# Kernel tuning notes

Measured on AMD Instinct MI355X. Metric: run time of the kernel, lower is better.

Reference implementation:

```python
import jax, jax.numpy as jnp
import numpy as np


def setup_inputs() -> dict:
    key = jax.random.key(0)
    N, E, H, V, C, D, L = 10000, 50000, 128, 8, 5, 59, 2
    keys = iter(jax.random.split(key, 64))

    def p(*shape):
        return jax.random.normal(next(keys), shape, jnp.float32) * 0.05

    inp = dict(
        edge_index=jax.random.randint(next(keys), (2, E), 0, N),
        edge_attr=jax.random.normal(next(keys), (E, D), jnp.float32),
        delta_t=jnp.array([60.0], jnp.float32),
        memory=jnp.ones((N, H), jnp.float32),
        # edge_embed
        W_ee=p(H, D), b_ee=p(H),
        # edge_weight_gen
        W_ewg=p(V, 2 * H), b_ewg=p(V),
        # multi-view GIN convs (L layers, shared MLP across views)
        gin_W1=p(L, H, H), gin_b1=p(L, H), gin_W2=p(L, H, H), gin_b2=p(L, H),
        # Bochner time encoder
        W_t=p(H, 1), b_t=p(H),
        # GRUCell (torch gate order r,z,n)
        W_ih=p(3 * H, H), b_ih=p(3 * H), W_hh=p(3 * H, H), b_hh=p(3 * H),
        # update_nn (feeds detached memory only; not in returned outputs)
        W_up=p(H, V * H), b_up=p(H),
        # local attention (kdim=vdim=2H, 1 head)
        Wq_l=p(H, H), bq_l=p(H), Wk_l=p(H, 2 * H), bk_l=p(H),
        Wv_l=p(H, 2 * H), bv_l=p(H), Wo_l=p(H, H), bo_l=p(H),
        # global attention (1 head)
        Wq_g=p(H, H), bq_g=p(H), Wk_g=p(H, H), bk_g=p(H),
        Wv_g=p(H, H), bv_g=p(H), Wo_g=p(H, H), bo_g=p(H),
        # classifier MLP
        Wc1=p(H, 3 * H), bc1=p(H), Wc2=p(C, H), bc2=p(C),
    )
    return inp


def reference(edge_index, edge_attr, delta_t, memory,
              W_ee, b_ee, W_ewg, b_ewg,
              gin_W1, gin_b1, gin_W2, gin_b2,
              W_t, b_t, W_ih, b_ih, W_hh, b_hh, W_up, b_up,
              Wq_l, bq_l, Wk_l, bk_l, Wv_l, bv_l, Wo_l, bo_l,
              Wq_g, bq_g, Wk_g, bk_g, Wv_g, bv_g, Wo_g, bo_g,
              Wc1, bc1, Wc2, bc2):
    relu = jax.nn.relu
    N, H = memory.shape
    V = W_ewg.shape[0]
    L = gin_W1.shape[0]

    # ---- snapshot encoder (MultiGraphLayer) ----
    ea = relu(edge_attr @ W_ee.T + b_ee)                               # [E,H]
    src0, dst0 = edge_index[0], edge_index[1]
    ew = jax.nn.sigmoid(
        jnp.concatenate([ea, memory[src0]], -1) @ W_ewg.T + b_ewg)     # [E,V]
    h = jnp.broadcast_to(memory[:, None, :], (N, V, H))                # [N,V,H]
    cs, cd = dst0, src0  # edge_index flipped before convs (edge_index[[1,0]])
    for l in range(L):
        # multi-view GIN: view-weighted message + residual MLP update
        msg = relu(h[cs] + ea[:, None, :]) * ew[:, :, None]            # [E,V,H]
        agg = jax.ops.segment_sum(msg, cd, num_segments=N)             # [N,V,H]
        upd = relu((h + agg) @ gin_W1[l].T + gin_b1[l]) @ gin_W2[l].T + gin_b2[l]
        h = h + upd
    h_before = h

    # ---- GRU memory update (vectorized over the V 'class' slots) ----
    te = jnp.sin(delta_t[:, None] * W_t[:, 0] + b_t)                   # [1,H]
    x_in = h + te                                                      # [N,V,H]
    gi = x_in @ W_ih.T + b_ih                                          # [N,V,3H]
    gh = (memory @ W_hh.T + b_hh)[:, None, :]                          # [N,1,3H]
    r = jax.nn.sigmoid(gi[..., :H] + gh[..., :H])
    z = jax.nn.sigmoid(gi[..., H:2 * H] + gh[..., H:2 * H])
    n = jnp.tanh(gi[..., 2 * H:] + r * gh[..., 2 * H:])
    h_new = (1.0 - z) * n + z * memory[:, None, :]                     # [N,V,H]

    # ---- global/local attention fusion ----
    scale = 1.0 / jnp.sqrt(jnp.asarray(H, jnp.float32))
    sf, df = h_new[src0], h_new[dst0]                                  # [E,V,H]
    Wk1, Wk2 = Wk_l[:, :H], Wk_l[:, H:]  # split cat([src,dst]) projection
    Wv1, Wv2 = Wv_l[:, :H], Wv_l[:, H:]
    q_l = ea @ Wq_l.T + bq_l                                           # [E,H]
    K_l = sf @ Wk1.T + df @ Wk2.T + bk_l                               # [E,V,H]
    V_l = sf @ Wv1.T + df @ Wv2.T + bv_l
    a_l = jax.nn.softmax(jnp.einsum('eh,evh->ev', q_l, K_l) * scale, -1)
    local_out = jnp.einsum('ev,evh->eh', a_l, V_l) @ Wo_l.T + bo_l     # [E,H]

    pooled = h_new.mean(axis=0)                                        # [V,H]
    q_g = ea @ Wq_g.T + bq_g
    K_g = pooled @ Wk_g.T + bk_g
    V_g = pooled @ Wv_g.T + bv_g
    a_g = jax.nn.softmax((q_g @ K_g.T) * scale, axis=-1)               # [E,V]
    global_out = (a_g @ V_g) @ Wo_g.T + bo_g                           # [E,H]

    combined = jnp.concatenate([ea, local_out, global_out], axis=-1)   # [E,3H]
    logits = relu(combined @ Wc1.T + bc1) @ Wc2.T + bc2                # [E,C]
    return (logits, ew, h_before, a_g[:, None, :])
```

## Files before the change

kernel.cpp:

```cpp
#include <hip/hip_runtime.h>
#include <cstddef>


#define HSZ 128
typedef unsigned short ushortT;
typedef unsigned int uintT;
typedef short short8 __attribute__((ext_vector_type(8)));
typedef float f32x4 __attribute__((ext_vector_type(4)));

__device__ __forceinline__ float sigm(float x) { return 1.f / (1.f + __expf(-x)); }

__device__ __forceinline__ ushortT f2bf(float f) {
  unsigned int u = __float_as_uint(f);
  u += 0x7fffu + ((u >> 16) & 1u);
  return (ushortT)(u >> 16);
}
__device__ __forceinline__ float bf2f(ushortT u) {
  return __uint_as_float(((unsigned int)u) << 16);
}
__device__ __forceinline__ float bflo(uintT u) { return __uint_as_float(u << 16); }
__device__ __forceinline__ float bfhi(uintT u) { return __uint_as_float(u & 0xffff0000u); }
__device__ __forceinline__ uintT pk2bf(float a, float b) {
  return ((uintT)f2bf(b) << 16) | (uintT)f2bf(a);
}

__device__ __forceinline__ int swzA(int row, int chunk) {
  return row * 64 + (((chunk ^ row) & 7) << 3);
}
__device__ __forceinline__ int swzT(int row, int chunk) {
  return row * 128 + (((chunk & 8) | ((chunk ^ row) & 7)) << 3);
}

template<int ASRC, int ACT, bool OUTBF, bool ABF, bool WBF>
__global__ __launch_bounds__(256) void gemm_bf(
    const void* __restrict__ A1, const void* __restrict__ A2, const void* __restrict__ A3,
    const void* __restrict__ W, const float* __restrict__ bias,
    void* __restrict__ out_, int M, int K, int Nout)
{
  __shared__ short Ash[128 * 64];
  __shared__ short Bsh[128 * 64];
  float* out = (float*)out_;
  ushortT* outh = (ushortT*)out_;
  const int tid = threadIdx.x;
  const int m0 = blockIdx.x * 128;
  const int n0 = blockIdx.y * 128;
  const int l = tid & 63, w = tid >> 6;
  const int wr = w >> 1, wc = w & 1;
  const int lr = l & 15, lq = l >> 4;
  f32x4 acc[4][4] = {};

  for (int k0 = 0; k0 < K; k0 += 64) {
    __syncthreads();
    const bool fast = (k0 + 64 <= K);
    #pragma unroll
    for (int i = 0; i < 4; ++i) {
      int c = i * 256 + tid;
      int row = c >> 3, seg = c & 7;
      int kb = k0 + seg * 8;
      {
        int m = m0 + row;
        short8 pk;
        if (ABF) {
          if (m < M) {
            if (ASRC == 4) {
              if (kb < 128)
                pk = *reinterpret_cast<const short8*>((const ushortT*)A1 + (size_t)m * 128 + kb);
              else if (kb < 384)
                pk = *reinterpret_cast<const short8*>((const ushortT*)A2 + (size_t)m * 256 + (kb - 128));
              else
                pk = *reinterpret_cast<const short8*>((const ushortT*)A3 + (size_t)m * 128 + (kb - 384));
            } else {
              pk = *reinterpret_cast<const short8*>((const ushortT*)A1 + (size_t)m * K + kb);
            }
          } else {
            #pragma unroll
            for (int j = 0; j < 8; ++j) pk[j] = 0;
          }
        } else {
          const float* A1f = (const float*)A1;
          float v[8];
          if (fast && m < M) {
            const float4* p = reinterpret_cast<const float4*>(A1f + (size_t)m * K + kb);
            float4 x0 = p[0], x1 = p[1];
            v[0]=x0.x; v[1]=x0.y; v[2]=x0.z; v[3]=x0.w;
            v[4]=x1.x; v[5]=x1.y; v[6]=x1.z; v[7]=x1.w;
          } else {
            #pragma unroll
            for (int j = 0; j < 8; ++j) {
              int k = kb + j;
              v[j] = (m < M && k < K) ? A1f[(size_t)m * K + k] : 0.f;
            }
          }
          #pragma unroll
          for (int j = 0; j < 8; ++j) pk[j] = (short)f2bf(v[j]);
        }
        *reinterpret_cast<short8*>(&Ash[swzA(row, seg)]) = pk;
      }
      {
        int nn = n0 + row;
        short8 pk;
        if (WBF) {
          if (nn < Nout)
            pk = *reinterpret_cast<const short8*>((const ushortT*)W + (size_t)nn * K + kb);
          else {
            #pragma unroll
            for (int j = 0; j < 8; ++j) pk[j] = 0;
          }
        } else {
          const float* Wf = (const float*)W;
          float v[8];
          if (fast && nn < Nout) {
            const float4* p = reinterpret_cast<const float4*>(Wf + (size_t)nn * K + kb);
            float4 x0 = p[0], x1 = p[1];
            v[0]=x0.x; v[1]=x0.y; v[2]=x0.z; v[3]=x0.w;
            v[4]=x1.x; v[5]=x1.y; v[6]=x1.z; v[7]=x1.w;
          } else {
            #pragma unroll
            for (int j = 0; j < 8; ++j) {
              int k = kb + j;
              v[j] = (nn < Nout && k < K) ? Wf[(size_t)nn * K + k] : 0.f;
            }
          }
          #pragma unroll
          for (int j = 0; j < 8; ++j) pk[j] = (short)f2bf(v[j]);
        }
        *reinterpret_cast<short8*>(&Bsh[swzA(row, seg)]) = pk;
      }
    }
    __syncthreads();
    #pragma unroll
    for (int ks = 0; ks < 2; ++ks) {
      short8 a[4], b[4];
      #pragma unroll
      for (int mi = 0; mi < 4; ++mi)
        a[mi] = *reinterpret_cast<const short8*>(&Ash[swzA(wr*64 + mi*16 + lr, ks*4 + lq)]);
      #pragma unroll
      for (int ni = 0; ni < 4; ++ni)
        b[ni] = *reinterpret_cast<const short8*>(&Bsh[swzA(wc*64 + ni*16 + lr, ks*4 + lq)]);
      #pragma unroll
      for (int mi = 0; mi < 4; ++mi)
        #pragma unroll
        for (int ni = 0; ni < 4; ++ni)
          acc[mi][ni] = __builtin_amdgcn_mfma_f32_16x16x32_bf16(a[mi], b[ni], acc[mi][ni], 0, 0, 0);
    }
  }
  #pragma unroll
  for (int ni = 0; ni < 4; ++ni) {
    int col = n0 + wc*64 + ni*16 + lr;
    if (col >= Nout) continue;
    float bz = bias ? bias[col] : 0.f;
    #pragma unroll
    for (int mi = 0; mi < 4; ++mi) {
      int mb = m0 + wr*64 + mi*16 + lq*4;
      #pragma unroll
      for (int r = 0; r < 4; ++r) {
        int m = mb + r;
        if (m >= M) continue;
        float vv = acc[mi][ni][r] + bz;
        if (ACT == 1) vv = fmaxf(vv, 0.f);
        size_t o = (size_t)m * Nout + col;
        if (OUTBF) outh[o] = f2bf(vv); else out[o] = vv;
      }
    }
  }
}

template<int LMODE>
__global__ __launch_bounds__(256) void k_gin(
    const ushortT* __restrict__ hb, const ushortT* __restrict__ aggb,
    float* __restrict__ houtf, ushortT* __restrict__ houtb,
    const ushortT* __restrict__ W1b, const float* __restrict__ b1,
    const ushortT* __restrict__ W2b, const float* __restrict__ b2, int M)
{
  __shared__ short smem[24576];
  short* Ash  = smem;
  short* Bsh  = smem + 8192;
  short* Tsh  = smem;
  short* B2sh = smem + 16384;
  const int tid = threadIdx.x;
  const int m0 = blockIdx.x * 128;
  const int l = tid & 63, w = tid >> 6;
  const int wr = w >> 1, wc = w & 1;
  const int lr = l & 15, lq = l >> 4;
  f32x4 acc[4][4] = {};

  for (int ks2 = 0; ks2 < 2; ++ks2) {
    if (ks2) __syncthreads();
    #pragma unroll
    for (int i = 0; i < 4; ++i) {
      int c = i * 256 + tid;
      int row = c >> 3, seg = c & 7;
      int kb = ks2 * 64 + seg * 8;
      {
        int m = m0 + row;
        short8 pk;
        if (m < M) {
          short8 hv;
          if (LMODE == 1) hv = *reinterpret_cast<const short8*>(hb + ((size_t)(m >> 3)) * 128 + kb);
          else            hv = *reinterpret_cast<const short8*>(hb + (size_t)m * 128 + kb);
          short8 av = *reinterpret_cast<const short8*>(aggb + (size_t)m * 128 + kb);
          #pragma unroll
          for (int j = 0; j < 8; ++j)
            pk[j] = (short)f2bf(bf2f((ushortT)hv[j]) + bf2f((ushortT)av[j]));
        } else {
          #pragma unroll
          for (int j = 0; j < 8; ++j) pk[j] = 0;
        }
        *reinterpret_cast<short8*>(&Ash[swzA(row, seg)]) = pk;
      }
      *reinterpret_cast<short8*>(&Bsh[swzA(row, seg)]) =
          *reinterpret_cast<const short8*>(W1b + (size_t)row * 128 + kb);
      if (ks2 == 0)
        *reinterpret_cast<short8*>(&B2sh[swzA(row, seg)]) =
            *reinterpret_cast<const short8*>(W2b + (size_t)row * 128 + seg * 8);
    }
    __syncthreads();
    #pragma unroll
    for (int ks = 0; ks < 2; ++ks) {
      short8 a[4], b[4];
      #pragma unroll
      for (int mi = 0; mi < 4; ++mi)
        a[mi] = *reinterpret_cast<const short8*>(&Ash[swzA(wr*64 + mi*16 + lr, ks*4 + lq)]);
      #pragma unroll
      for (int ni = 0; ni < 4; ++ni)
        b[ni] = *reinterpret_cast<const short8*>(&Bsh[swzA(wc*64 + ni*16 + lr, ks*4 + lq)]);
      #pragma unroll
      for (int mi = 0; mi < 4; ++mi)
        #pragma unroll
        for (int ni = 0; ni < 4; ++ni)
          acc[mi][ni] = __builtin_amdgcn_mfma_f32_16x16x32_bf16(a[mi], b[ni], acc[mi][ni], 0, 0, 0);
    }
  }
  __syncthreads();
  {
    float b1v[4];
    #pragma unroll
    for (int ni = 0; ni < 4; ++ni) b1v[ni] = b1[wc*64 + ni*16 + lr];
    #pragma unroll
    for (int mi = 0; mi < 4; ++mi)
      #pragma unroll
      for (int ni = 0; ni < 4; ++ni) {
        int col = wc*64 + ni*16 + lr;
        #pragma unroll
        for (int r = 0; r < 4; ++r) {
          int row = wr*64 + mi*16 + lq*4 + r;
          float v = fmaxf(acc[mi][ni][r] + b1v[ni], 0.f);
          Tsh[swzT(row, col >> 3) + (col & 7)] = (short)f2bf(v);
        }
      }
  }
  __syncthreads();
  f32x4 acc2[4][4] = {};
  for (int ks2 = 0; ks2 < 2; ++ks2) {
    if (ks2) {
      __syncthreads();
      #pragma unroll
      for (int i = 0; i < 4; ++i) {
        int c = i * 256 + tid;
        int row = c >> 3, seg = c & 7;
        *reinterpret_cast<short8*>(&B2sh[swzA(row, seg)]) =
            *reinterpret_cast<const short8*>(W2b + (size_t)row * 128 + 64 + seg * 8);
      }
      __syncthreads();
    }
    #pragma unroll
    for (int ks = 0; ks < 2; ++ks) {
      short8 a[4], b[4];
      #pragma unroll
      for (int mi = 0; mi < 4; ++mi)
        a[mi] = *reinterpret_cast<const short8*>(&Tsh[swzT(wr*64 + mi*16 + lr, ks2*8 + ks*4 + lq)]);
      #pragma unroll
      for (int ni = 0; ni < 4; ++ni)
        b[ni] = *reinterpret_cast<const short8*>(&B2sh[swzA(wc*64 + ni*16 + lr, ks*4 + lq)]);
      #pragma unroll
      for (int mi = 0; mi < 4; ++mi)
        #pragma unroll
        for (int ni = 0; ni < 4; ++ni)
          acc2[mi][ni] = __builtin_amdgcn_mfma_f32_16x16x32_bf16(a[mi], b[ni], acc2[mi][ni], 0, 0, 0);
    }
  }
  {
    float b2v[4];
    #pragma unroll
    for (int ni = 0; ni < 4; ++ni) b2v[ni] = b2[wc*64 + ni*16 + lr];
    #pragma unroll
    for (int ni = 0; ni < 4; ++ni) {
      int col = wc*64 + ni*16 + lr;
      #pragma unroll
      for (int mi = 0; mi < 4; ++mi) {
        int mb = m0 + wr*64 + mi*16 + lq*4;
        #pragma unroll
        for (int r = 0; r < 4; ++r) {
          int m = mb + r;
          if (m >= M) continue;
          float base = (LMODE == 1) ? bf2f(hb[((size_t)(m >> 3)) * 128 + col])
                                    : bf2f(hb[(size_t)m * 128 + col]);
          float ho = base + acc2[mi][ni][r] + b2v[ni];
          if (LMODE == 1) houtb[(size_t)m * 128 + col] = f2bf(ho);
          else            houtf[(size_t)m * 128 + col] = ho;
        }
      }
    }
  }
}

__global__ __launch_bounds__(512) void k_giru(
    const float* __restrict__ hf, const float* __restrict__ te,
    const ushortT* __restrict__ Wihb, const float* __restrict__ b_ih,
    const ushortT* __restrict__ ghb, const ushortT* __restrict__ memb,
    ushortT* __restrict__ hnb, float* __restrict__ prw, int M)
{
  __shared__ short Ash[8192];
  __shared__ short Bsh[24576];
  float* poolsh = reinterpret_cast<float*>(Ash);
  const int tid = threadIdx.x;
  const int m0 = blockIdx.x * 64;
  const int l = tid & 63, w = tid >> 6;
  const int lr = l & 15, lq = l >> 4;
  const int r0 = (w >> 1) * 16, c0 = (w & 1) * 64;
  f32x4 acc[3][4] = {};

  #pragma unroll
  for (int i = 0; i < 2; ++i) {
    int c = i * 512 + tid;
    int row = c >> 4, seg = c & 15;
    int m = m0 + row;
    short8 pk;
    if (m < M) {
      const float4* p = reinterpret_cast<const float4*>(hf + (size_t)m * 128 + seg * 8);
      const float4* t = reinterpret_cast<const float4*>(te + seg * 8);
      float4 x0 = p[0], x1 = p[1], t0 = t[0], t1 = t[1];
      pk[0]=(short)f2bf(x0.x+t0.x); pk[1]=(short)f2bf(x0.y+t0.y);
      pk[2]=(short)f2bf(x0.z+t0.z); pk[3]=(short)f2bf(x0.w+t0.w);
      pk[4]=(short)f2bf(x1.x+t1.x); pk[5]=(short)f2bf(x1.y+t1.y);
      pk[6]=(short)f2bf(x1.z+t1.z); pk[7]=(short)f2bf(x1.w+t1.w);
    } else {
      #pragma unroll
      for (int j = 0; j < 8; ++j) pk[j] = 0;
    }
    *reinterpret_cast<short8*>(&Ash[swzT(row, seg)]) = pk;
  }
  for (int ks2 = 0; ks2 < 2; ++ks2) {
    if (ks2) __syncthreads();
    #pragma unroll
    for (int i = 0; i < 6; ++i) {
      int c = i * 512 + tid;
      int row = c >> 3, seg = c & 7;
      *reinterpret_cast<short8*>(&Bsh[swzA(row, seg)]) =
          *reinterpret_cast<const short8*>(Wihb + (size_t)row * 128 + ks2 * 64 + seg * 8);
    }
    __syncthreads();
    #pragma unroll
    for (int ks = 0; ks < 2; ++ks) {
      short8 a = *reinterpret_cast<const short8*>(&Ash[swzT(r0 + lr, ks2*8 + ks*4 + lq)]);
      #pragma unroll
      for (int s = 0; s < 3; ++s)
        #pragma unroll
        for (int xi = 0; xi < 4; ++xi) {
          short8 b = *reinterpret_cast<const short8*>(
              &Bsh[swzA(s*128 + c0 + xi*16 + lr, ks*4 + lq)]);
          acc[s][xi] = __builtin_amdgcn_mfma_f32_16x16x32_bf16(a, b, acc[s][xi], 0, 0, 0);
        }
    }
  }
  __syncthreads();
  for (int i = tid; i < 1024; i += 512) poolsh[i] = 0.f;
  __syncthreads();
  #pragma unroll
  for (int xi = 0; xi < 4; ++xi) {
    int x = c0 + xi * 16 + lr;
    float br = b_ih[x], bz = b_ih[128 + x], bn = b_ih[256 + x];
    #pragma unroll
    for (int rr = 0; rr < 4; ++rr) {
      int m = m0 + r0 + lq * 4 + rr;
      if (m >= M) continue;
      int node = m >> 3;
      float ghr = bf2f(ghb[(size_t)node * 384 + x]);
      float ghz = bf2f(ghb[(size_t)node * 384 + 128 + x]);
      float ghn = bf2f(ghb[(size_t)node * 384 + 256 + x]);
      float mem = bf2f(memb[(size_t)node * 128 + x]);
      float rv = sigm(acc[0][xi][rr] + br + ghr);
      float zv = sigm(acc[1][xi][rr] + bz + ghz);
      float nv = tanhf(acc[2][xi][rr] + bn + rv * ghn);
      float hn = (1.f - zv) * nv + zv * mem;
      hnb[(size_t)m * 128 + x] = f2bf(hn);
      atomicAdd(&poolsh[(m & 7) * 128 + x], hn);
    }
  }
  __syncthreads();
  for (int i = tid; i < 1024; i += 512) atomicAdd(&prw[i], poolsh[i]);
}

__global__ void k_hist(const int* __restrict__ srcI, int* __restrict__ cnt, int E)
{
  int e = blockIdx.x * 256 + threadIdx.x;
  if (e < E) atomicAdd(&cnt[srcI[e]], 1);
}

__global__ __launch_bounds__(1024) void k_scan(const int* __restrict__ cnt,
    int* __restrict__ ofs, int* __restrict__ cur, int N)
{
  __shared__ int buf[1024];
  __shared__ int carry;
  int tid = threadIdx.x;
  if (tid == 0) carry = 0;
  __syncthreads();
  for (int base = 0; base < N; base += 1024) {
    int i = base + tid;
    int v = (i < N) ? cnt[i] : 0;
    buf[tid] = v;
    __syncthreads();
    for (int off = 1; off < 1024; off <<= 1) {
      int t = (tid >= off) ? buf[tid - off] : 0;
      __syncthreads();
      buf[tid] += t;
      __syncthreads();
    }
    int excl = carry + buf[tid] - v;
    if (i < N) { ofs[i] = excl; cur[i] = excl; }
    __syncthreads();
    if (tid == 0) carry += buf[1023];
    __syncthreads();
  }
  if (tid == 0) ofs[N] = carry;
}

__global__ void k_fill(const int* __restrict__ srcI, int* __restrict__ cur,
                       int* __restrict__ eid, int E)
{
  int e = blockIdx.x * 256 + threadIdx.x;
  if (e >= E) return;
  int p = atomicAdd(&cur[srcI[e]], 1);
  eid[p] = e;
}

template<int LMODE>
__global__ __launch_bounds__(256) void k_agg(const ushortT* __restrict__ hb,
    const ushortT* __restrict__ eab, const float* __restrict__ ew,
    const int* __restrict__ dstI, const int* __restrict__ ofs,
    const int* __restrict__ eid, ushortT* __restrict__ aggb, int N)
{
  int half = threadIdx.x >> 7;
  int x = threadIdx.x & 127;
  int n = blockIdx.x * 2 + half;
  if (n >= N) return;
  float acc[8] = {};
  int beg = ofs[n], end = ofs[n + 1];
  for (int i = beg; i < end; ++i) {
    int e = eid[i];
    int d = dstI[e];
    float eav = bf2f(eab[(size_t)e * 128 + x]);
    const float* ewp = ew + (size_t)e * 8;
    if (LMODE == 1) {
      float m = fmaxf(bf2f(hb[(size_t)d * 128 + x]) + eav, 0.f);
      #pragma unroll
      for (int v = 0; v < 8; ++v) acc[v] += m * ewp[v];
    } else {
      const ushortT* hd = hb + (size_t)d * 1024;
      #pragma unroll
      for (int v = 0; v < 8; ++v)
        acc[v] += fmaxf(bf2f(hd[v * 128 + x]) + eav, 0.f) * ewp[v];
    }
  }
  ushortT* ag = aggb + (size_t)n * 1024;
  #pragma unroll
  for (int v = 0; v < 8; ++v) ag[v * 128 + x] = f2bf(acc[v]);
}

__global__ __launch_bounds__(256) void k_ew(const ushortT* __restrict__ eab,
    const ushortT* __restrict__ memb, const int* __restrict__ srcI,
    const float* __restrict__ W_ewg, const float* __restrict__ b_ewg,
    float* __restrict__ ew, int E)
{
  __shared__ float Wsh[2048];
  __shared__ float bsh[8];
  int tid = threadIdx.x;
  for (int i = tid; i < 2048; i += 256) Wsh[i] = W_ewg[i];
  if (tid < 8) bsh[tid] = b_ewg[tid];
  __syncthreads();
  int wv = tid >> 6, lane = tid & 63;
  int e = blockIdx.x * 4 + wv;
  if (e >= E) return;
  int s = srcI[e];
  float c0 = bf2f(eab[(size_t)e * 128 + lane]);
  float c1 = bf2f(eab[(size_t)e * 128 + 64 + lane]);
  float c2 = bf2f(memb[(size_t)s * 128 + lane]);
  float c3 = bf2f(memb[(size_t)s * 128 + 64 + lane]);
  #pragma unroll
  for (int v = 0; v < 8; ++v) {
    float p = c0 * Wsh[v * 256 + lane] + c1 * Wsh[v * 256 + 64 + lane]
            + c2 * Wsh[v * 256 + 128 + lane] + c3 * Wsh[v * 256 + 192 + lane];
    #pragma unroll
    for (int o = 32; o; o >>= 1) p += __shfl_down(p, o);
    if (lane == 0) ew[(size_t)e * 8 + v] = sigm(p + bsh[v]);
  }
}

__global__ void k_cvtall(const float* __restrict__ s0, ushortT* __restrict__ d0, int n0,
                         const float* __restrict__ s1, ushortT* __restrict__ d1, int n1,
                         const float* __restrict__ s2, ushortT* __restrict__ d2, int n2,
                         const float* __restrict__ s3, ushortT* __restrict__ d3, int n3)
{
  int i = blockIdx.x * 256 + threadIdx.x;
  if (i < n0) { d0[i] = f2bf(s0[i]); return; }
  i -= n0;
  if (i < n1) { d1[i] = f2bf(s1[i]); return; }
  i -= n1;
  if (i < n2) { d2[i] = f2bf(s2[i]); return; }
  i -= n2;
  if (i < n3) d3[i] = f2bf(s3[i]);
}

__global__ __launch_bounds__(256) void k_prep(
    const float* __restrict__ Wo_l, const float* __restrict__ Wv_l,
    const float* __restrict__ bv_l, const float* __restrict__ bo_l,
    const float* __restrict__ Wq_l, const float* __restrict__ bq_l,
    const float* __restrict__ Wk_l,
    const float* __restrict__ delta_t, const float* __restrict__ W_t,
    const float* __restrict__ b_t,
    float* __restrict__ Wl2f, float* __restrict__ blv,
    ushortT* __restrict__ Wqkgb, float* __restrict__ bqkg, float* __restrict__ te)
{
  int idx = blockIdx.x * 256 + threadIdx.x;
  if (idx < 32768) {
    int n = idx >> 8, k = idx & 255;
    float a = 0.f;
    for (int j = 0; j < 128; ++j) a += Wo_l[n * 128 + j] * Wv_l[j * 256 + k];
    Wl2f[idx] = a;
  } else {
    int rem = idx - 32768;
    int n = rem >> 7, j = rem & 127;
    float a = 0.f;
    for (int k = 0; k < 128; ++k) a += Wq_l[k * 128 + j] * Wk_l[k * 256 + n];
    Wqkgb[rem] = f2bf(a);
  }
  if (blockIdx.x == 0 && threadIdx.x < 128) {
    int n = threadIdx.x;
    float a = bo_l[n];
    for (int j = 0; j < 128; ++j) a += Wo_l[n * 128 + j] * bv_l[j];
    blv[n] = a;
  }
  if (blockIdx.x == 1) {
    int n = threadIdx.x;
    float a = 0.f;
    for (int k = 0; k < 128; ++k) a += bq_l[k] * Wk_l[k * 256 + n];
    bqkg[n] = a;
  }
  if (blockIdx.x == 2 && threadIdx.x < 128) {
    int t = threadIdx.x;
    te[t] = sinf(delta_t[0] * W_t[t] + b_t[t]);
  }
}

__global__ __launch_bounds__(256) void k_prep2(
    const float* __restrict__ Wc1, const float* __restrict__ bc1,
    const float* __restrict__ Wl2f, const float* __restrict__ blv,
    ushortT* __restrict__ Wc1p, float* __restrict__ bc1p)
{
  int idx = blockIdx.x * 256 + threadIdx.x;
  int n = idx >> 9, k = idx & 511;
  float a;
  if (k < 128) a = Wc1[(size_t)n * 384 + k];
  else if (k < 384) {
    int kk = k - 128;
    a = 0.f;
    for (int j = 0; j < 128; ++j) a += Wc1[(size_t)n * 384 + 128 + j] * Wl2f[j * 256 + kk];
  } else a = Wc1[(size_t)n * 384 + 256 + (k - 384)];
  Wc1p[idx] = f2bf(a);
  if (blockIdx.x == 0 && threadIdx.x < 128) {
    int nn = threadIdx.x;
    float b = bc1[nn];
    for (int j = 0; j < 128; ++j) b += Wc1[(size_t)nn * 384 + 128 + j] * blv[j];
    bc1p[nn] = b;
  }
}

__global__ __launch_bounds__(256) void k_kgg(const float* __restrict__ prw,
    const float* __restrict__ Wk_g, const float* __restrict__ Wv_g, const float* __restrict__ bv_g,
    const float* __restrict__ Wo_g, float* __restrict__ Kg, float* __restrict__ G, int N)
{
  __shared__ float pl[1024];
  __shared__ float vg[1024];
  int tid = threadIdx.x;
  float invN = 1.f / (float)N;
  for (int i = tid; i < 1024; i += 256) pl[i] = prw[i] * invN;
  __syncthreads();
  for (int o = tid; o < 1024; o += 256) {
    int v = o >> 7, x = o & 127;
    float a = 0.f, b = 0.f;
    for (int k = 0; k < 128; ++k) {
      float p = pl[v * 128 + k];
      a += p * Wk_g[(size_t)x * 128 + k];
      b += p * Wv_g[(size_t)x * 128 + k];
    }
    Kg[o] = a;
    vg[o] = b + bv_g[x];
  }
  __syncthreads();
  for (int o = tid; o < 1024; o += 256) {
    int v = o >> 7, x = o & 127;
    float a = 0.f;
    for (int k = 0; k < 128; ++k) a += vg[v * 128 + k] * Wo_g[(size_t)x * 128 + k];
    G[o] = a;
  }
}

__global__ __launch_bounds__(256) void k_sc(const float* __restrict__ Kg,
    const float* __restrict__ Wq_g, const float* __restrict__ bq_g,
    ushortT* __restrict__ Wqkgb, float* __restrict__ bqkg)
{
  int idx = blockIdx.x * 256 + threadIdx.x;
  int v = idx >> 7, j = idx & 127;
  float a = 0.f;
  for (int x = 0; x < 128; ++x) a += Kg[v * 128 + x] * Wq_g[(size_t)x * 128 + j];
  Wqkgb[(size_t)(256 + v) * 128 + j] = f2bf(a);
  if (blockIdx.x == 0 && threadIdx.x < 8) {
    int vv = threadIdx.x;
    float b = 0.f;
    for (int x = 0; x < 128; ++x) b += bq_g[x] * Kg[vv * 128 + x];
    bqkg[256 + vv] = b;
  }
}

__global__ __launch_bounds__(256) void k_lg(
    const ushortT* __restrict__ hnb, const ushortT* __restrict__ qkgb,
    const int* __restrict__ srcI, const int* __restrict__ dstI,
    const float* __restrict__ G, const float* __restrict__ bo_g,
    float* __restrict__ ag_out, ushortT* __restrict__ wsd,
    ushortT* __restrict__ glbb, int E)
{
  __shared__ float Gs[1024], bsh[128];
  int tid = threadIdx.x;
  for (int i = tid; i < 1024; i += 256) Gs[i] = G[i];
  if (tid < 128) bsh[tid] = bo_g[tid];
  __syncthreads();
  int w = tid >> 6, l = tid & 63, half = l >> 5, l31 = l & 31;
  int e = blockIdx.x * 8 + w * 2 + half;
  int ec = (e < E) ? e : (E - 1);
  int s = srcI[ec], d = dstI[ec];
  const uint2* qrow = reinterpret_cast<const uint2*>(qkgb + (size_t)ec * 264);
  uint2 q1u = qrow[l31], q2u = qrow[32 + l31];
  uint4 scu = *reinterpret_cast<const uint4*>(qkgb + (size_t)ec * 264 + 256);
  const uint2* srow = reinterpret_cast<const uint2*>(hnb + (size_t)s * 1024);
  const uint2* drow = reinterpret_cast<const uint2*>(hnb + (size_t)d * 1024);
  uint2 su[8], du[8];
  #pragma unroll
  for (int v = 0; v < 8; ++v) { su[v] = srow[v * 32 + l31]; du[v] = drow[v * 32 + l31]; }
  float q1f[4] = {bflo(q1u.x), bfhi(q1u.x), bflo(q1u.y), bfhi(q1u.y)};
  float q2f[4] = {bflo(q2u.x), bfhi(q2u.x), bflo(q2u.y), bfhi(q2u.y)};
  float pl[8];
  #pragma unroll
  for (int v = 0; v < 8; ++v) {
    pl[v] = q1f[0] * bflo(su[v].x) + q1f[1] * bfhi(su[v].x)
          + q1f[2] * bflo(su[v].y) + q1f[3] * bfhi(su[v].y)
          + q2f[0] * bflo(du[v].x) + q2f[1] * bfhi(du[v].x)
          + q2f[2] * bflo(du[v].y) + q2f[3] * bfhi(du[v].y);
  }
  #pragma unroll
  for (int v = 0; v < 8; ++v) {
    #pragma unroll
    for (int m = 1; m <= 16; m <<= 1) pl[v] += __shfl_xor(pl[v], m);
  }
  const float scale = 0.08838834764831845f;
  float mx = fmaxf(fmaxf(fmaxf(pl[0], pl[1]), fmaxf(pl[2], pl[3])),
                   fmaxf(fmaxf(pl[4], pl[5]), fmaxf(pl[6], pl[7])));
  float suml = 0.f, al[8];
  #pragma unroll
  for (int v = 0; v < 8; ++v) { al[v] = __expf((pl[v] - mx) * scale); suml += al[v]; }
  float invl = 1.f / suml;
  float ws0 = 0.f, ws1 = 0.f, ws2 = 0.f, ws3 = 0.f;
  float wd0 = 0.f, wd1 = 0.f, wd2 = 0.f, wd3 = 0.f;
  #pragma unroll
  for (int v = 0; v < 8; ++v) {
    float a = al[v];
    ws0 += a * bflo(su[v].x); ws1 += a * bfhi(su[v].x);
    ws2 += a * bflo(su[v].y); ws3 += a * bfhi(su[v].y);
    wd0 += a * bflo(du[v].x); wd1 += a * bfhi(du[v].x);
    wd2 += a * bflo(du[v].y); wd3 += a * bfhi(du[v].y);
  }
  if (e < E) {
    uint2* wrow = reinterpret_cast<uint2*>(wsd + (size_t)e * 256);
    uint2 t0; t0.x = pk2bf(ws0 * invl, ws1 * invl); t0.y = pk2bf(ws2 * invl, ws3 * invl);
    uint2 t1; t1.x = pk2bf(wd0 * invl, wd1 * invl); t1.y = pk2bf(wd2 * invl, wd3 * invl);
    wrow[l31] = t0;
    wrow[32 + l31] = t1;
  }
  float sg[8] = {bflo(scu.x), bfhi(scu.x), bflo(scu.y), bfhi(scu.y),
                 bflo(scu.z), bfhi(scu.z), bflo(scu.w), bfhi(scu.w)};
  float mg = fmaxf(fmaxf(fmaxf(sg[0], sg[1]), fmaxf(sg[2], sg[3])),
                   fmaxf(fmaxf(sg[4], sg[5]), fmaxf(sg[6], sg[7])));
  float sumg = 0.f, ag[8];
  #pragma unroll
  for (int v = 0; v < 8; ++v) { ag[v] = __expf((sg[v] - mg) * scale); sumg += ag[v]; }
  float invg = 1.f / sumg;
  if (e < E && l31 < 8) ag_out[(size_t)e * 8 + l31] = ag[l31] * invg;
  float4 b4 = *reinterpret_cast<const float4*>(&bsh[4 * l31]);
  float g0 = b4.x, g1 = b4.y, g2 = b4.z, g3 = b4.w;
  #pragma unroll
  for (int v = 0; v < 8; ++v) {
    float sv = ag[v] * invg;
    float4 gv = *reinterpret_cast<const float4*>(&Gs[v * 128 + 4 * l31]);
    g0 += sv * gv.x; g1 += sv * gv.y; g2 += sv * gv.z; g3 += sv * gv.w;
  }
  if (e < E) {
    uint2 t; t.x = pk2bf(g0, g1); t.y = pk2bf(g2, g3);
    reinterpret_cast<uint2*>(glbb + (size_t)e * 128)[l31] = t;
  }
}

__global__ __launch_bounds__(256) void k_logits(const ushortT* __restrict__ hid,
    const float* __restrict__ Wc2, const float* __restrict__ bc2,
    float* __restrict__ logits, int E)
{
  __shared__ float Wsh[640];
  __shared__ float bsh[5];
  int tid = threadIdx.x;
  for (int i = tid; i < 640; i += 256) Wsh[i] = Wc2[i];
  if (tid < 5) bsh[tid] = bc2[tid];
  __syncthreads();
  int wv = tid >> 6, lane = tid & 63;
  int e = blockIdx.x * 4 + wv;
  if (e >= E) return;
  float h0 = bf2f(hid[(size_t)e * 128 + lane]), h1 = bf2f(hid[(size_t)e * 128 + 64 + lane]);
  #pragma unroll
  for (int c = 0; c < 5; ++c) {
    float p = h0 * Wsh[c * 128 + lane] + h1 * Wsh[c * 128 + 64 + lane];
    #pragma unroll
    for (int o = 32; o; o >>= 1) p += __shfl_down(p, o);
    if (lane == 0) logits[(size_t)e * 5 + c] = p + bsh[c];
  }
}

extern "C" void kernel_launch(void* const* d_in, const int* in_sizes, int n_in,
                              void* d_out, int out_size, void* d_ws, size_t ws_size,
                              hipStream_t stream)
{
  const int*   edge_index = (const int*)d_in[0];
  const float* edge_attr  = (const float*)d_in[1];
  const float* delta_t    = (const float*)d_in[2];
  const float* memory     = (const float*)d_in[3];
  const float* W_ee  = (const float*)d_in[4];
  const float* b_ee  = (const float*)d_in[5];
  const float* W_ewg = (const float*)d_in[6];
  const float* b_ewg = (const float*)d_in[7];
  const float* gin_W1 = (const float*)d_in[8];
  const float* gin_b1 = (const float*)d_in[9];
  const float* gin_W2 = (const float*)d_in[10];
  const float* gin_b2 = (const float*)d_in[11];
  const float* W_t  = (const float*)d_in[12];
  const float* b_t  = (const float*)d_in[13];
  const float* W_ih = (const float*)d_in[14];
  const float* b_ih = (const float*)d_in[15];
  const float* W_hh = (const float*)d_in[16];
  const float* b_hh = (const float*)d_in[17];
  const float* Wq_l = (const float*)d_in[20];
  const float* bq_l = (const float*)d_in[21];
  const float* Wk_l = (const float*)d_in[22];
  const float* Wv_l = (const float*)d_in[24];
  const float* bv_l = (const float*)d_in[25];
  const float* Wo_l = (const float*)d_in[26];
  const float* bo_l = (const float*)d_in[27];
  const float* Wq_g = (const float*)d_in[28];
  const float* bq_g = (const float*)d_in[29];
  const float* Wk_g = (const float*)d_in[30];
  const float* Wv_g = (const float*)d_in[32];
  const float* bv_g = (const float*)d_in[33];
  const float* Wo_g = (const float*)d_in[34];
  const float* bo_g = (const float*)d_in[35];
  const float* Wc1  = (const float*)d_in[36];
  const float* bc1  = (const float*)d_in[37];
  const float* Wc2  = (const float*)d_in[38];
  const float* bc2  = (const float*)d_in[39];

  const int E = in_sizes[0] / 2;
  const int N = in_sizes[3] / HSZ;
  const int* srcI = edge_index;
  const int* dstI = edge_index + E;

  float* out    = (float*)d_out;
  float* logits = out;
  float* ew     = out + (size_t)E * 5;
  float* h      = out + (size_t)E * 13;
  float* ag_out = out + (size_t)E * 13 + (size_t)N * 1024;

  float* ws = (float*)d_ws;
  size_t off = 0;
  auto alloc = [&](size_t n) { size_t o = off; off += (n + 255) & ~(size_t)255; return o; };
  float* te   = ws + alloc(128);
  float* blv  = ws + alloc(128);
  float* bqkg = ws + alloc(384);
  float* bc1p = ws + alloc(128);
  float* Kg   = ws + alloc(1024);
  float* G    = ws + alloc(1024);
  float* prw  = ws + alloc(1024);
  int* cnt = (int*)(ws + alloc(N));
  int* ofs = (int*)(ws + alloc(N + 1));
  int* cur = (int*)(ws + alloc(N));
  int* eid = (int*)(ws + alloc(E));
  ushortT* memb   = (ushortT*)(ws + alloc((size_t)N * 64));
  ushortT* eab    = (ushortT*)(ws + alloc((size_t)E * 64));
  ushortT* h1b    = (ushortT*)(ws + alloc((size_t)N * 512));
  ushortT* hnb    = (ushortT*)(ws + alloc((size_t)N * 512));
  ushortT* ghb    = (ushortT*)(ws + alloc((size_t)N * 192));
  ushortT* ginW1b = (ushortT*)(ws + alloc(16384));
  ushortT* ginW2b = (ushortT*)(ws + alloc(16384));
  ushortT* Wihb   = (ushortT*)(ws + alloc(24576));
  float*   Wl2f   = ws + alloc(32768);
  ushortT* Wc1p   = (ushortT*)(ws + alloc(32768));
  ushortT* Wqkgb  = (ushortT*)(ws + alloc(16896));
  size_t brA = (size_t)N * 512, brC = (size_t)E * 324;
  size_t brsz = brA > brC ? brA : brC;
  float* BR = ws + alloc(brsz);
  if (ws_size < off * sizeof(float)) return;

  ushortT* aggb = (ushortT*)BR;
  ushortT* qkgb = (ushortT*)BR;
  ushortT* wsd  = (ushortT*)(BR + (size_t)E * 132);
  ushortT* glbb = (ushortT*)(BR + (size_t)E * 260);
  ushortT* hid  = (ushortT*)BR;

  auto cdiv = [](int a, int b) { return (a + b - 1) / b; };

  hipMemsetAsync(cnt, 0, (size_t)N * sizeof(int), stream);
  hipMemsetAsync(prw, 0, 1024 * sizeof(float), stream);
  k_hist<<<cdiv(E, 256), 256, 0, stream>>>(srcI, cnt, E);
  k_scan<<<1, 1024, 0, stream>>>(cnt, ofs, cur, N);
  k_fill<<<cdiv(E, 256), 256, 0, stream>>>(srcI, cur, eid, E);
  {
    int total = N * 128 + 32768 + 32768 + 49152;
    k_cvtall<<<cdiv(total, 256), 256, 0, stream>>>(
        memory, memb, N * 128, gin_W1, ginW1b, 32768,
        gin_W2, ginW2b, 32768, W_ih, Wihb, 49152);
  }
  gemm_bf<0, 1, true, false, false><<<dim3(cdiv(E, 128), 1), 256, 0, stream>>>(
      edge_attr, nullptr, nullptr, W_ee, b_ee, eab, E, 59, 128);
  k_ew<<<cdiv(E, 4), 256, 0, stream>>>(eab, memb, srcI, W_ewg, b_ewg, ew, E);
  k_prep<<<256, 256, 0, stream>>>(Wo_l, Wv_l, bv_l, bo_l, Wq_l, bq_l, Wk_l,
                                  delta_t, W_t, b_t, Wl2f, blv, Wqkgb, bqkg, te);
  k_prep2<<<256, 256, 0, stream>>>(Wc1, bc1, Wl2f, blv, Wc1p, bc1p);
  gemm_bf<0, 0, true, false, false><<<dim3(cdiv(N, 128), 3), 256, 0, stream>>>(
      memory, nullptr, nullptr, W_hh, b_hh, ghb, N, 128, 384);
  k_agg<1><<<cdiv(N, 2), 256, 0, stream>>>(memb, eab, ew, dstI, ofs, eid, aggb, N);
  k_gin<1><<<cdiv(N * 8, 128), 256, 0, stream>>>(
      memb, aggb, nullptr, h1b, ginW1b, gin_b1, ginW2b, gin_b2, N * 8);
  k_agg<2><<<cdiv(N, 2), 256, 0, stream>>>(h1b, eab, ew, dstI, ofs, eid, aggb, N);
  k_gin<2><<<cdiv(N * 8, 128), 256, 0, stream>>>(
      h1b, aggb, h, nullptr, ginW1b + 16384, gin_b1 + 128,
      ginW2b + 16384, gin_b2 + 128, N * 8);
  k_giru<<<cdiv(N * 8, 64), 512, 0, stream>>>(h, te, Wihb, b_ih, ghb, memb, hnb, prw, N * 8);
  k_kgg<<<1, 256, 0, stream>>>(prw, Wk_g, Wv_g, bv_g, Wo_g, Kg, G, N);
  k_sc<<<4, 256, 0, stream>>>(Kg, Wq_g, bq_g, Wqkgb, bqkg);
  gemm_bf<0, 0, true, true, true><<<dim3(cdiv(E, 128), 3), 256, 0, stream>>>(
      eab, nullptr, nullptr, Wqkgb, bqkg, qkgb, E, 128, 264);
  k_lg<<<cdiv(E, 8), 256, 0, stream>>>(hnb, qkgb, srcI, dstI, G, bo_g,
                                       ag_out, wsd, glbb, E);
  gemm_bf<4, 1, true, true, true><<<dim3(cdiv(E, 128), 1), 256, 0, stream>>>(
      eab, wsd, glbb, Wc1p, bc1p, hid, E, 512, 128);
  k_logits<<<cdiv(E, 4), 256, 0, stream>>>(hid, Wc2, bc2, logits, E);
}
```

Measured before the change: 535.5 us.

## Load GEMM operands directly from global into registers, dropping LDS staging

In the GIN MLP and GRU input-projection kernels, A and weight (B) fragments are now read straight from global memory into MFMA registers instead of being staged through shared memory. This removes several __syncthreads barriers and cuts LDS use, which can allow more resident blocks. In exchange, each wave re-reads the weights from global/L2 in a less coalesced pattern, and the GIN A operand (h+agg) is recomputed per wave instead of being shared.

```diff
diff --git a/kernel.cpp b/kernel.cpp
--- a/kernel.cpp
+++ b/kernel.cpp
@@ -172,11 +172,7 @@
     const ushortT* __restrict__ W1b, const float* __restrict__ b1,
     const ushortT* __restrict__ W2b, const float* __restrict__ b2, int M)
 {
-  __shared__ short smem[24576];
-  short* Ash  = smem;
-  short* Bsh  = smem + 8192;
-  short* Tsh  = smem;
-  short* B2sh = smem + 16384;
+  __shared__ short Tsh[16384];
   const int tid = threadIdx.x;
   const int m0 = blockIdx.x * 128;
   const int l = tid & 63, w = tid >> 6;
@@ -184,54 +180,35 @@
   const int lr = l & 15, lq = l >> 4;
   f32x4 acc[4][4] = {};
 
-  for (int ks2 = 0; ks2 < 2; ++ks2) {
-    if (ks2) __syncthreads();
-    #pragma unroll
-    for (int i = 0; i < 4; ++i) {
-      int c = i * 256 + tid;
-      int row = c >> 3, seg = c & 7;
-      int kb = ks2 * 64 + seg * 8;
-      {
-        int m = m0 + row;
-        short8 pk;
-        if (m < M) {
-          short8 hv;
-          if (LMODE == 1) hv = *reinterpret_cast<const short8*>(hb + ((size_t)(m >> 3)) * 128 + kb);
-          else            hv = *reinterpret_cast<const short8*>(hb + (size_t)m * 128 + kb);
-          short8 av = *reinterpret_cast<const short8*>(aggb + (size_t)m * 128 + kb);
-          #pragma unroll
-          for (int j = 0; j < 8; ++j)
-            pk[j] = (short)f2bf(bf2f((ushortT)hv[j]) + bf2f((ushortT)av[j]));
-        } else {
-          #pragma unroll
-          for (int j = 0; j < 8; ++j) pk[j] = 0;
-        }
-        *reinterpret_cast<short8*>(&Ash[swzA(row, seg)]) = pk;
+  #pragma unroll
+  for (int kk = 0; kk < 4; ++kk) {
+    const int kof = kk * 32 + lq * 8;
+    short8 a[4], b[4];
+    #pragma unroll
+    for (int mi = 0; mi < 4; ++mi) {
+      int m = m0 + wr*64 + mi*16 + lr;
+      if (m < M) {
+        short8 hv;
+        if (LMODE == 1) hv = *reinterpret_cast<const short8*>(hb + ((size_t)(m >> 3)) * 128 + kof);
+        else            hv = *reinterpret_cast<const short8*>(hb + (size_t)m * 128 + kof);
+        short8 av = *reinterpret_cast<const short8*>(aggb + (size_t)m * 128 + kof);
+        #pragma unroll
+        for (int j = 0; j < 8; ++j)
+          a[mi][j] = (short)f2bf(bf2f((ushortT)hv[j]) + bf2f((ushortT)av[j]));
+      } else {
+        #pragma unroll
+        for (int j = 0; j < 8; ++j) a[mi][j] = 0;
       }
-      *reinterpret_cast<short8*>(&Bsh[swzA(row, seg)]) =
-          *reinterpret_cast<const short8*>(W1b + (size_t)row * 128 + kb);
-      if (ks2 == 0)
-        *reinterpret_cast<short8*>(&B2sh[swzA(row, seg)]) =
-            *reinterpret_cast<const short8*>(W2b + (size_t)row * 128 + seg * 8);
-    }
-    __syncthreads();
-    #pragma unroll
-    for (int ks = 0; ks < 2; ++ks) {
-      short8 a[4], b[4];
-      #pragma unroll
-      for (int mi = 0; mi < 4; ++mi)
-        a[mi] = *reinterpret_cast<const short8*>(&Ash[swzA(wr*64 + mi*16 + lr, ks*4 + lq)]);
+    }
+    #pragma unroll
+    for (int ni = 0; ni < 4; ++ni)
+      b[ni] = *reinterpret_cast<const short8*>(W1b + (size_t)(wc*64 + ni*16 + lr) * 128 + kof);
+    #pragma unroll
+    for (int mi = 0; mi < 4; ++mi)
       #pragma unroll
       for (int ni = 0; ni < 4; ++ni)
-        b[ni] = *reinterpret_cast<const short8*>(&Bsh[swzA(wc*64 + ni*16 + lr, ks*4 + lq)]);
-      #pragma unroll
-      for (int mi = 0; mi < 4; ++mi)
-        #pragma unroll
-        for (int ni = 0; ni < 4; ++ni)
-          acc[mi][ni] = __builtin_amdgcn_mfma_f32_16x16x32_bf16(a[mi], b[ni], acc[mi][ni], 0, 0, 0);
-    }
-  }
-  __syncthreads();
+        acc[mi][ni] = __builtin_amdgcn_mfma_f32_16x16x32_bf16(a[mi], b[ni], acc[mi][ni], 0, 0, 0);
+  }
   {
     float b1v[4];
     #pragma unroll
@@ -251,33 +228,21 @@
   }
   __syncthreads();
   f32x4 acc2[4][4] = {};
-  for (int ks2 = 0; ks2 < 2; ++ks2) {
-    if (ks2) {
-      __syncthreads();
-      #pragma unroll
-      for (int i = 0; i < 4; ++i) {
-        int c = i * 256 + tid;
-        int row = c >> 3, seg = c & 7;
-        *reinterpret_cast<short8*>(&B2sh[swzA(row, seg)]) =
-            *reinterpret_cast<const short8*>(W2b + (size_t)row * 128 + 64 + seg * 8);
-      }
-      __syncthreads();
-    }
-    #pragma unroll
-    for (int ks = 0; ks < 2; ++ks) {
-      short8 a[4], b[4];
-      #pragma unroll
-      for (int mi = 0; mi < 4; ++mi)
-        a[mi] = *reinterpret_cast<const short8*>(&Tsh[swzT(wr*64 + mi*16 + lr, ks2*8 + ks*4 + lq)]);
+  #pragma unroll
+  for (int kk = 0; kk < 4; ++kk) {
+    const int kof = kk * 32 + lq * 8;
+    short8 a[4], b[4];
+    #pragma unroll
+    for (int mi = 0; mi < 4; ++mi)
+      a[mi] = *reinterpret_cast<const short8*>(&Tsh[swzT(wr*64 + mi*16 + lr, kk*4 + lq)]);
+    #pragma unroll
+    for (int ni = 0; ni < 4; ++ni)
+      b[ni] = *reinterpret_cast<const short8*>(W2b + (size_t)(wc*64 + ni*16 + lr) * 128 + kof);
+    #pragma unroll
+    for (int mi = 0; mi < 4; ++mi)
       #pragma unroll
       for (int ni = 0; ni < 4; ++ni)
-        b[ni] = *reinterpret_cast<const short8*>(&B2sh[swzA(wc*64 + ni*16 + lr, ks*4 + lq)]);
-      #pragma unroll
-      for (int mi = 0; mi < 4; ++mi)
-        #pragma unroll
-        for (int ni = 0; ni < 4; ++ni)
-          acc2[mi][ni] = __builtin_amdgcn_mfma_f32_16x16x32_bf16(a[mi], b[ni], acc2[mi][ni], 0, 0, 0);
-    }
+        acc2[mi][ni] = __builtin_amdgcn_mfma_f32_16x16x32_bf16(a[mi], b[ni], acc2[mi][ni], 0, 0, 0);
   }
   {
     float b2v[4];
@@ -311,8 +276,7 @@
     ushortT* __restrict__ hnb, float* __restrict__ prw, int M)
 {
   __shared__ short Ash[8192];
-  __shared__ short Bsh[24576];
-  float* poolsh = reinterpret_cast<float*>(Ash);
+  __shared__ float poolsh[1024];
   const int tid = threadIdx.x;
   const int m0 = blockIdx.x * 64;
   const int l = tid & 63, w = tid >> 6;
@@ -340,32 +304,20 @@
     }
     *reinterpret_cast<short8*>(&Ash[swzT(row, seg)]) = pk;
   }
-  for (int ks2 = 0; ks2 < 2; ++ks2) {
-    if (ks2) __syncthreads();
-    #pragma unroll
-    for (int i = 0; i < 6; ++i) {
-      int c = i * 512 + tid;
-      int row = c >> 3, seg = c & 7;
-      *reinterpret_cast<short8*>(&Bsh[swzA(row, seg)]) =
-          *reinterpret_cast<const short8*>(Wihb + (size_t)row * 128 + ks2 * 64 + seg * 8);
-    }
-    __syncthreads();
-    #pragma unroll
-    for (int ks = 0; ks < 2; ++ks) {
-      short8 a = *reinterpret_cast<const short8*>(&Ash[swzT(r0 + lr, ks2*8 + ks*4 + lq)]);
-      #pragma unroll
-      for (int s = 0; s < 3; ++s)
-        #pragma unroll
-        for (int xi = 0; xi < 4; ++xi) {
-          short8 b = *reinterpret_cast<const short8*>(
-              &Bsh[swzA(s*128 + c0 + xi*16 + lr, ks*4 + lq)]);
-          acc[s][xi] = __builtin_amdgcn_mfma_f32_16x16x32_bf16(a, b, acc[s][xi], 0, 0, 0);
-        }
-    }
-  }
-  __syncthreads();
   for (int i = tid; i < 1024; i += 512) poolsh[i] = 0.f;
   __syncthreads();
+  #pragma unroll
+  for (int kk = 0; kk < 4; ++kk) {
+    short8 a = *reinterpret_cast<const short8*>(&Ash[swzT(r0 + lr, kk*4 + lq)]);
+    #pragma unroll
+    for (int s = 0; s < 3; ++s)
+      #pragma unroll
+      for (int xi = 0; xi < 4; ++xi) {
+        short8 b = *reinterpret_cast<const short8*>(
+            Wihb + (size_t)(s*128 + c0 + xi*16 + lr) * 128 + kk*32 + lq*8);
+        acc[s][xi] = __builtin_amdgcn_mfma_f32_16x16x32_bf16(a, b, acc[s][xi], 0, 0, 0);
+      }
+  }
   #pragma unroll
   for (int xi = 0; xi < 4; ++xi) {
     int x = c0 + xi * 16 + lr;
```

Measured after the change: 562.3 us. +5.0%, slower.
